# Kernel tuning notes

Measured on AMD Instinct MI355X. Metric: run time of the kernel, lower is better.

The kernel has to match this reference:

```python
import math
import jax, jax.numpy as jnp
import numpy as np

DIM = 1024
HID = 2048  # dim * expansion_factor
QK = 128
G = 256  # group size
NUM_BUCKETS = 32
MAX_DIST = 128
SCALE = QK ** 0.5


def t5_rel_bias(rel_emb, g):
    # non-causal T5 relative position bias over a g x g window
    pos = jnp.arange(g)
    n = pos[:, None] - pos[None, :]  # n = -(k - q) = q - k
    nb = NUM_BUCKETS // 2  # 16
    ret = (n < 0).astype(jnp.int32) * nb
    n = jnp.abs(n)
    max_exact = nb // 2  # 8
    is_small = n < max_exact
    val_large = max_exact + (
        jnp.log(jnp.maximum(n, 1).astype(jnp.float32) / max_exact)
        / math.log(MAX_DIST / max_exact) * (nb - max_exact)
    ).astype(jnp.int32)
    val_large = jnp.minimum(val_large, nb - 1)
    bucket = ret + jnp.where(is_small, n, val_large)
    return rel_emb[bucket, 0] * SCALE  # [g, g]


def setup_inputs() -> dict:
    key = jax.random.key(0)
    ks = jax.random.split(key, 8)
    d = {}
    d['x'] = jax.random.normal(ks[0], (4, 4096, DIM), dtype=jnp.float32)
    d['ln_g'] = jnp.ones((DIM,), jnp.float32)
    d['ln_b'] = jnp.zeros((DIM,), jnp.float32)
    d['W_h'] = jax.random.normal(ks[1], (DIM, 2 * HID), jnp.float32) * (1.0 / math.sqrt(DIM))
    d['b_h'] = jnp.zeros((2 * HID,), jnp.float32)
    d['W_qk'] = jax.random.normal(ks[2], (DIM, QK), jnp.float32) * (1.0 / math.sqrt(DIM))
    d['b_qk'] = jnp.zeros((QK,), jnp.float32)
    d['os_g'] = 1.0 + 0.02 * jax.random.normal(ks[3], (4, QK), jnp.float32)
    d['os_b'] = jnp.zeros((4, QK), jnp.float32)
    d['rel_emb'] = jax.random.normal(ks[4], (NUM_BUCKETS, 1), jnp.float32)
    d['W_o'] = jax.random.normal(ks[5], (HID, DIM), jnp.float32) * (1.0 / math.sqrt(HID))
    d['b_o'] = jnp.zeros((DIM,), jnp.float32)
    return d


def reference(x, ln_g, ln_b, W_h, b_h, W_qk, b_qk, os_g, os_b, rel_emb, W_o, b_o):
    b, n, _ = x.shape
    # LayerNorm
    mu = jnp.mean(x, axis=-1, keepdims=True)
    var = jnp.var(x, axis=-1, keepdims=True)
    normed = (x - mu) * jax.lax.rsqrt(var + 1e-5) * ln_g + ln_b
    # to_hidden -> v, gate ; to_qk
    hidden = jax.nn.silu(normed @ W_h + b_h)  # [b, n, 2*HID]
    v, gate = hidden[..., :HID], hidden[..., HID:]
    qk = jax.nn.silu(normed @ W_qk + b_qk)  # [b, n, QK]
    # offset-scale into 4 heads
    heads = qk[..., None, :] * os_g + os_b  # [b, n, 4, QK]
    quad_q, lin_q, quad_k, lin_k = [heads[..., h, :] for h in range(4)]
    # group: n divisible by G (no padding needed)
    ng = n // G
    grp = lambda t: t.reshape(b, ng, G, -1)
    quad_q, quad_k, lin_q, lin_k, vg = map(grp, (quad_q, quad_k, lin_q, lin_k, v))
    # grouped quadratic attention with ReLU^2 and T5 bias
    sim = jnp.einsum('bgid,bgjd->bgij', quad_q, quad_k) / G
    sim = sim + t5_rel_bias(rel_emb, G)
    attn = jnp.square(jax.nn.relu(sim))
    quad_out = jnp.einsum('bgij,bgjd->bgid', attn, vg)
    # linear attention, reduced over groups (non-causal)
    lin_kv = jnp.einsum('bgnd,bgne->bde', lin_k, vg) / n
    lin_out = jnp.einsum('bgnd,bde->bgne', lin_q, lin_kv)
    out = gate * (quad_out.reshape(b, n, HID) + lin_out.reshape(b, n, HID))
    return out @ W_o + b_o + x
```

## Files before the change

### kernel.cpp

```cpp
#include <hip/hip_runtime.h>
#include <hip/hip_bf16.h>

typedef float  f32x4  __attribute__((ext_vector_type(4)));
typedef __bf16 bf16x8 __attribute__((ext_vector_type(8)));
typedef __bf16 bf16x4 __attribute__((ext_vector_type(4)));

__device__ __forceinline__ float silu_f(float x) { return x / (1.0f + __expf(-x)); }

__device__ __forceinline__ void gload16(const __bf16* g, const char* lds) {
    __builtin_amdgcn_global_load_lds((const __attribute__((address_space(1))) void*)g,
                                     (__attribute__((address_space(3))) void*)lds, 16, 0, 0);
}

__global__ __launch_bounds__(256) void prepln_kernel(const float* __restrict__ x,
                                                     const float* __restrict__ ln_g,
                                                     const float* __restrict__ ln_b,
                                                     __bf16* __restrict__ norm,
                                                     const float* __restrict__ W_h,
                                                     const float* __restrict__ W_qk,
                                                     const float* __restrict__ W_o,
                                                     const float* __restrict__ rel_emb,
                                                     __bf16* __restrict__ WhT,
                                                     __bf16* __restrict__ WqkT,
                                                     __bf16* __restrict__ WoT,
                                                     float* __restrict__ bmat) {
    __shared__ float red[8];
    __shared__ __bf16 tile[32][33];
    int id = blockIdx.x, tid = threadIdx.x;
    if (id < 16384) {
        const float* xr = x + (long)id * 1024;
        f32x4 v = *(const f32x4*)(xr + tid * 4);
        float s  = v[0] + v[1] + v[2] + v[3];
        float ss = v[0]*v[0] + v[1]*v[1] + v[2]*v[2] + v[3]*v[3];
        #pragma unroll
        for (int off = 32; off > 0; off >>= 1) {
            s  += __shfl_down(s, off);
            ss += __shfl_down(ss, off);
        }
        int wave = tid >> 6, lane = tid & 63;
        if (lane == 0) { red[wave*2] = s; red[wave*2+1] = ss; }
        __syncthreads();
        float S  = red[0] + red[2] + red[4] + red[6];
        float SS = red[1] + red[3] + red[5] + red[7];
        float mean = S * (1.0f/1024.0f);
        float var  = SS * (1.0f/1024.0f) - mean*mean;
        float rstd = rsqrtf(var + 1e-5f);
        __bf16* orow = norm + (long)id * 1024;
        #pragma unroll
        for (int j = 0; j < 4; j++) {
            float fv = (v[j] - mean) * rstd * ln_g[tid*4+j] + ln_b[tid*4+j];
            orow[tid*4+j] = (__bf16)fv;
        }
        return;
    }
    id -= 16384;
    if (id >= 6272) {
        int idx = (id - 6272) * 256 + tid;
        int i = idx >> 8, j = idx & 255;
        int n = i - j;
        int ret = (n < 0) ? 16 : 0;
        int an = (n < 0) ? -n : n;
        int bucket;
        if (an < 8) {
            bucket = ret + an;
        } else {
            float vl = logf((float)an * 0.125f) / 2.772588722239781f * 8.0f;
            int lv = 8 + (int)vl;
            bucket = ret + (lv < 15 ? lv : 15);
        }
        bmat[idx] = rel_emb[bucket] * 11.313708498984761f;
        return;
    }
    const float* in; __bf16* outp; int rows, cols, tx, ty;
    if (id < 4096)      { in = W_h;  outp = WhT;  rows = 1024; cols = 4096; tx = id % 128; ty = id / 128; }
    else if (id < 4224) { int t = id - 4096; in = W_qk; outp = WqkT; rows = 1024; cols = 128;  tx = t % 4;  ty = t / 4; }
    else                { int t = id - 4224; in = W_o;  outp = WoT;  rows = 2048; cols = 1024; tx = t % 32; ty = t / 32; }
    int c0 = tx * 32, r0 = ty * 32;
    int lx = tid & 31, ly = tid >> 5;
    #pragma unroll
    for (int i = 0; i < 4; i++) {
        int r = ly + i*8;
        tile[r][lx] = (__bf16)in[(long)(r0 + r) * cols + c0 + lx];
    }
    __syncthreads();
    #pragma unroll
    for (int i = 0; i < 4; i++) {
        int c = ly + i*8;
        outp[(long)(c0 + c) * rows + r0 + lx] = tile[lx][c];
    }
}

__global__ __launch_bounds__(256) void reduce8_kernel(const __bf16* __restrict__ in,
                                                      __bf16* __restrict__ out) {
    int i = (blockIdx.x * 256 + threadIdx.x) * 4;
    int b = i >> 18;
    int r = i & 262143;
    float s0 = 0.f, s1 = 0.f, s2 = 0.f, s3 = 0.f;
    #pragma unroll
    for (int c = 0; c < 8; ++c) {
        bf16x4 v = *(const bf16x4*)(in + ((long)(b*8 + c) << 18) + r);
        s0 += (float)v[0]; s1 += (float)v[1]; s2 += (float)v[2]; s3 += (float)v[3];
    }
    bf16x4 o; o[0] = (__bf16)s0; o[1] = (__bf16)s1; o[2] = (__bf16)s2; o[3] = (__bf16)s3;
    *(bf16x4*)(out + i) = o;
}

struct GP {
    const __bf16* A;
    const __bf16* B;
    const __bf16* A2;
    const __bf16* B2;
    int lda, ldb, kSteps;
    long sAz, sBz, sCz;
    float scale;
    float* outF;
    __bf16 *o0, *o1, *o2, *o3, *o4, *o5;
    const float *c0, *c1, *c2, *c3;
    __bf16* gbuf;
};

__global__ __launch_bounds__(256, 2) void hqk_kernel(GP p) {
    __shared__ __bf16 As[2*128*32];
    __shared__ __bf16 Bs[2*128*32];
    int bx = blockIdx.x, by = blockIdx.y;
    bool qkm = (by == 32);
    const __bf16* A = p.A + (long)bx * 128 * 1024;
    const __bf16* B = qkm ? p.B2 : p.B + (long)by * 128 * 1024;
    int tid = threadIdx.x;
    int wave = tid >> 6, lane = tid & 63;
    int wr = (wave >> 1) * 64, wc = (wave & 1) * 64;
    int lr = lane & 15, kg = lane >> 4;

    f32x4 acc[4][4] = {};

    int lsub = lane >> 2;
    int scol = (lane & 3) * 8;
    const __bf16* Ag = A + scol + (long)(wave*32 + lsub) * 1024;
    const __bf16* Bg = B + scol + (long)(wave*32 + lsub) * 1024;
    const long s16 = 16 * 1024;
    __bf16* AsW = As + wave * 32 * 32;
    __bf16* BsW = Bs + wave * 32 * 32;

    for (int ks = 0; ks < 16; ++ks) {
        long k0 = (long)ks * 64;
        __syncthreads();
        gload16(Ag + k0,            (const char*)AsW);
        gload16(Ag + k0 + s16,      (const char*)(AsW + 16*32));
        gload16(Bg + k0,            (const char*)BsW);
        gload16(Bg + k0 + s16,      (const char*)(BsW + 16*32));
        gload16(Ag + k0 + 32,       (const char*)(AsW + 4096));
        gload16(Ag + k0 + 32 + s16, (const char*)(AsW + 4096 + 16*32));
        gload16(Bg + k0 + 32,       (const char*)(BsW + 4096));
        gload16(Bg + k0 + 32 + s16, (const char*)(BsW + 4096 + 16*32));
        __syncthreads();
#pragma unroll
        for (int kk = 0; kk < 2; ++kk) {
            bf16x8 af[4], bfr[4];
            #pragma unroll
            for (int i = 0; i < 4; i++) af[i]  = *(const bf16x8*)(As + kk*4096 + (wr + i*16 + lr)*32 + kg*8);
            #pragma unroll
            for (int i = 0; i < 4; i++) bfr[i] = *(const bf16x8*)(Bs + kk*4096 + (wc + i*16 + lr)*32 + kg*8);
            #pragma unroll
            for (int i = 0; i < 4; i++)
                #pragma unroll
                for (int j = 0; j < 4; j++)
                    acc[i][j] = __builtin_amdgcn_mfma_f32_16x16x32_bf16(af[i], bfr[j], acc[i][j], 0, 0, 0);
        }
    }

    #pragma unroll
    for (int i = 0; i < 4; i++) {
        #pragma unroll
        for (int j = 0; j < 4; j++) {
            int row0 = bx*128 + wr + i*16 + kg*4;
            if (!qkm) {
                int col = by*128 + wc + j*16 + lr;
                if (col < 2048) {
                    bf16x4 vv;
                    #pragma unroll
                    for (int q = 0; q < 4; q++) vv[q] = (__bf16)silu_f(acc[i][j][q] + p.c0[col]);
                    *(bf16x4*)(p.o0 + (long)col*16384 + row0) = vv;
                } else {
                    #pragma unroll
                    for (int q = 0; q < 4; q++)
                        p.o1[(long)(row0+q)*2048 + (col - 2048)] = (__bf16)silu_f(acc[i][j][q] + p.c0[col]);
                }
            } else {
                int col = wc + j*16 + lr;
                float sv[4];
                #pragma unroll
                for (int q = 0; q < 4; q++) sv[q] = silu_f(acc[i][j][q] + p.c3[col]);
                #pragma unroll
                for (int q = 0; q < 4; q++) {
                    p.o2[(long)(row0+q)*128 + col] = (__bf16)(sv[q] * p.c1[      col] + p.c2[      col]);
                    p.o3[(long)(row0+q)*128 + col] = (__bf16)(sv[q] * p.c1[256 + col] + p.c2[256 + col]);
                    p.o4[(long)(row0+q)*128 + col] = (__bf16)(sv[q] * p.c1[128 + col] + p.c2[128 + col]);
                }
                bf16x4 lk;
                #pragma unroll
                for (int q = 0; q < 4; q++) lk[q] = (__bf16)(sv[q] * p.c1[384 + col] + p.c2[384 + col]);
                *(bf16x4*)(p.o5 + (long)col*16384 + row0) = lk;
            }
        }
    }
}

__global__ __launch_bounds__(256, 2) void gemm64f_kernel(GP p) {
    __shared__ __bf16 As[2*128*32];
    __shared__ __bf16 Bs[2*128*32];
    const __bf16* A = p.A + (long)blockIdx.x * 128 * p.lda;
    const __bf16* B = p.B + (long)blockIdx.y * 128 * p.ldb;
    int tid = threadIdx.x;
    int wave = tid >> 6, lane = tid & 63;
    int wr = (wave >> 1) * 64, wc = (wave & 1) * 64;
    int lr = lane & 15, kg = lane >> 4;

    f32x4 acc[4][4] = {};

    int lsub = lane >> 2;
    int scol = (lane & 3) * 8;
    const __bf16* Ag = A + scol + (long)(wave*32 + lsub) * p.lda;
    const __bf16* Bg = B + scol + (long)(wave*32 + lsub) * p.ldb;
    long a16 = (long)16 * p.lda, b16 = (long)16 * p.ldb;
    __bf16* AsW = As + wave * 32 * 32;
    __bf16* BsW = Bs + wave * 32 * 32;

    for (int ks = 0; ks < p.kSteps; ++ks) {
        long k0 = (long)ks * 64;
        __syncthreads();
        gload16(Ag + k0,            (const char*)AsW);
        gload16(Ag + k0 + a16,      (const char*)(AsW + 16*32));
        gload16(Bg + k0,            (const char*)BsW);
        gload16(Bg + k0 + b16,      (const char*)(BsW + 16*32));
        gload16(Ag + k0 + 32,       (const char*)(AsW + 4096));
        gload16(Ag + k0 + 32 + a16, (const char*)(AsW + 4096 + 16*32));
        gload16(Bg + k0 + 32,       (const char*)(BsW + 4096));
        gload16(Bg + k0 + 32 + b16, (const char*)(BsW + 4096 + 16*32));
        __syncthreads();
#pragma unroll
        for (int kk = 0; kk < 2; ++kk) {
            bf16x8 af[4], bfr[4];
            #pragma unroll
            for (int i = 0; i < 4; i++) af[i]  = *(const bf16x8*)(As + kk*4096 + (wr + i*16 + lr)*32 + kg*8);
            #pragma unroll
            for (int i = 0; i < 4; i++) bfr[i] = *(const bf16x8*)(Bs + kk*4096 + (wc + i*16 + lr)*32 + kg*8);
            #pragma unroll
            for (int i = 0; i < 4; i++)
                #pragma unroll
                for (int j = 0; j < 4; j++)
                    acc[i][j] = __builtin_amdgcn_mfma_f32_16x16x32_bf16(af[i], bfr[j], acc[i][j], 0, 0, 0);
        }
    }

    int bx = blockIdx.x, by = blockIdx.y;
    #pragma unroll
    for (int i = 0; i < 4; i++) {
        #pragma unroll
        for (int j = 0; j < 4; j++) {
            int row0 = bx*128 + wr + i*16 + kg*4;
            int col  = by*128 + wc + j*16 + lr;
            #pragma unroll
            for (int q = 0; q < 4; q++) {
                long idx = (long)(row0+q)*1024 + col;
                p.outF[idx] = acc[i][j][q] + p.c0[col] + p.c1[idx];
            }
        }
    }
}

__global__ __launch_bounds__(256, 2) void simlinkv_kernel(GP ps, GP pl) {
    __shared__ __bf16 As[2*128*32];
    __shared__ __bf16 Bs[2*128*32];
    int id = blockIdx.x;
    bool sim = id < 256;
    GP p = sim ? ps : pl;
    int bx, by, z;
    if (sim) { bx = id & 1; by = (id >> 1) & 1; z = id >> 2; }
    else     { int t = id - 256; bx = 0; by = t & 15; z = t >> 4; }

    const __bf16* A = p.A + (long)z * p.sAz + (long)bx * 128 * p.lda;
    const __bf16* B = p.B + (long)z * p.sBz + (long)by * 128 * p.ldb;
    int tid = threadIdx.x;
    int wave = tid >> 6, lane = tid & 63;
    int wr = (wave >> 1) * 64, wc = (wave & 1) * 64;
    int lr = lane & 15, kg = lane >> 4;

    f32x4 acc[4][4] = {};

    int lsub = lane >> 2;
    int scol = (lane & 3) * 8;
    const __bf16* Ag = A + scol + (long)(wave*32 + lsub) * p.lda;
    const __bf16* Bg = B + scol + (long)(wave*32 + lsub) * p.ldb;
    long a16 = (long)16 * p.lda, b16 = (long)16 * p.ldb;
    __bf16* AsW = As + wave * 32 * 32;
    __bf16* BsW = Bs + wave * 32 * 32;

    for (int ks = 0; ks < p.kSteps; ++ks) {
        long k0 = (long)ks * 64;
        __syncthreads();
        gload16(Ag + k0,            (const char*)AsW);
        gload16(Ag + k0 + a16,      (const char*)(AsW + 16*32));
        gload16(Bg + k0,            (const char*)BsW);
        gload16(Bg + k0 + b16,      (const char*)(BsW + 16*32));
        gload16(Ag + k0 + 32,       (const char*)(AsW + 4096));
        gload16(Ag + k0 + 32 + a16, (const char*)(AsW + 4096 + 16*32));
        gload16(Bg + k0 + 32,       (const char*)(BsW + 4096));
        gload16(Bg + k0 + 32 + b16, (const char*)(BsW + 4096 + 16*32));
        __syncthreads();
#pragma unroll
        for (int kk = 0; kk < 2; ++kk) {
            bf16x8 af[4], bfr[4];
            #pragma unroll
            for (int i = 0; i < 4; i++) af[i]  = *(const bf16x8*)(As + kk*4096 + (wr + i*16 + lr)*32 + kg*8);
            #pragma unroll
            for (int i = 0; i < 4; i++) bfr[i] = *(const bf16x8*)(Bs + kk*4096 + (wc + i*16 + lr)*32 + kg*8);
            #pragma unroll
            for (int i = 0; i < 4; i++)
                #pragma unroll
                for (int j = 0; j < 4; j++)
                    acc[i][j] = __builtin_amdgcn_mfma_f32_16x16x32_bf16(af[i], bfr[j], acc[i][j], 0, 0, 0);
        }
    }

    #pragma unroll
    for (int i = 0; i < 4; i++) {
        #pragma unroll
        for (int j = 0; j < 4; j++) {
            int row0 = bx*128 + wr + i*16 + kg*4;
            int col  = by*128 + wc + j*16 + lr;
            if (sim) {
                #pragma unroll
                for (int q = 0; q < 4; q++) {
                    int row = row0 + q;
                    float s = acc[i][j][q] * (1.0f/256.0f) + p.c0[row*256 + col];
                    s = fmaxf(s, 0.0f);
                    p.o0[(long)z*p.sCz + (long)row*256 + col] = (__bf16)(s * s);
                }
            } else {
                bf16x4 vv;
                #pragma unroll
                for (int q = 0; q < 4; q++) vv[q] = (__bf16)(acc[i][j][q] * p.scale);
                *(bf16x4*)(p.o0 + (long)z*p.sCz + (long)col*128 + row0) = vv;
            }
        }
    }
}

__global__ __launch_bounds__(256, 2) void quadlin_kernel(GP p) {
    __shared__ __bf16 As[2*128*32];
    __shared__ __bf16 Bs[2*128*32];
    int z = blockIdx.z;
    int batch = z >> 4;
    int tid = threadIdx.x;
    int wave = tid >> 6, lane = tid & 63;
    int wr = (wave >> 1) * 64, wc = (wave & 1) * 64;
    int lr = lane & 15, kg = lane >> 4;
    int lsub = lane >> 2;
    int scol = (lane & 3) * 8;
    __bf16* AsW = As + wave * 32 * 32;
    __bf16* BsW = Bs + wave * 32 * 32;

    f32x4 acc[4][4] = {};

    {
        const __bf16* Ag = p.A + (long)z * 65536 + (long)blockIdx.x * 128 * 256
                         + scol + (long)(wave*32 + lsub) * 256;
        const __bf16* Bg = p.B + (long)z * 256 + (long)blockIdx.y * 128 * 16384
                         + scol + (long)(wave*32 + lsub) * 16384;
        const long a16 = 16*256, b16 = 16L*16384;
        for (int ks = 0; ks < 4; ++ks) {
            long k0 = (long)ks * 64;
            __syncthreads();
            gload16(Ag + k0,            (const char*)AsW);
            gload16(Ag + k0 + a16,      (const char*)(AsW + 16*32));
            gload16(Bg + k0,            (const char*)BsW);
            gload16(Bg + k0 + b16,      (const char*)(BsW + 16*32));
            gload16(Ag + k0 + 32,       (const char*)(AsW + 4096));
            gload16(Ag + k0 + 32 + a16, (const char*)(AsW + 4096 + 16*32));
            gload16(Bg + k0 + 32,       (const char*)(BsW + 4096));
            gload16(Bg + k0 + 32 + b16, (const char*)(BsW + 4096 + 16*32));
            __syncthreads();
#pragma unroll
            for (int kk = 0; kk < 2; ++kk) {
                bf16x8 af[4], bfr[4];
                #pragma unroll
                for (int i = 0; i < 4; i++) af[i]  = *(const bf16x8*)(As + kk*4096 + (wr + i*16 + lr)*32 + kg*8);
                #pragma unroll
                for (int i = 0; i < 4; i++) bfr[i] = *(const bf16x8*)(Bs + kk*4096 + (wc + i*16 + lr)*32 + kg*8);
                #pragma unroll
                for (int i = 0; i < 4; i++)
                    #pragma unroll
                    for (int j = 0; j < 4; j++)
                        acc[i][j] = __builtin_amdgcn_mfma_f32_16x16x32_bf16(af[i], bfr[j], acc[i][j], 0, 0, 0);
            }
        }
    }
    {
        const __bf16* Ag = p.A2 + ((long)z * 256 + (long)blockIdx.x * 128) * 128
                         + scol + (long)(wave*32 + lsub) * 128;
        const __bf16* Bg = p.B2 + (long)batch * 2048 * 128 + (long)blockIdx.y * 128 * 128
                         + scol + (long)(wave*32 + lsub) * 128;
        const long a16 = 16*128, b16 = 16*128;
        for (int ks = 0; ks < 2; ++ks) {
            long k0 = (long)ks * 64;
            __syncthreads();
            gload16(Ag + k0,            (const char*)AsW);
            gload16(Ag + k0 + a16,      (const char*)(AsW + 16*32));
            gload16(Bg + k0,            (const char*)BsW);
            gload16(Bg + k0 + b16,      (const char*)(BsW + 16*32));
            gload16(Ag + k0 + 32,       (const char*)(AsW + 4096));
            gload16(Ag + k0 + 32 + a16, (const char*)(AsW + 4096 + 16*32));
            gload16(Bg + k0 + 32,       (const char*)(BsW + 4096));
            gload16(Bg + k0 + 32 + b16, (const char*)(BsW + 4096 + 16*32));
            __syncthreads();
#pragma unroll
            for (int kk = 0; kk < 2; ++kk) {
                bf16x8 af[4], bfr[4];
                #pragma unroll
                for (int i = 0; i < 4; i++) af[i]  = *(const bf16x8*)(As + kk*4096 + (wr + i*16 + lr)*32 + kg*8);
                #pragma unroll
                for (int i = 0; i < 4; i++) bfr[i] = *(const bf16x8*)(Bs + kk*4096 + (wc + i*16 + lr)*32 + kg*8);
                #pragma unroll
                for (int i = 0; i < 4; i++)
                    #pragma unroll
                    for (int j = 0; j < 4; j++)
                        acc[i][j] = __builtin_amdgcn_mfma_f32_16x16x32_bf16(af[i], bfr[j], acc[i][j], 0, 0, 0);
            }
        }
    }
    #pragma unroll
    for (int i = 0; i < 4; i++) {
        #pragma unroll
        for (int j = 0; j < 4; j++) {
            int row0 = z*256 + blockIdx.x*128 + wr + i*16 + kg*4;
            int col  = blockIdx.y*128 + wc + j*16 + lr;
            #pragma unroll
            for (int q = 0; q < 4; q++) {
                long idx = (long)(row0+q)*2048 + col;
                float g = (float)p.gbuf[idx];
                p.gbuf[idx] = (__bf16)(g * acc[i][j][q]);
            }
        }
    }
}

extern "C" void kernel_launch(void* const* d_in, const int* in_sizes, int n_in,
                              void* d_out, int out_size, void* d_ws, size_t ws_size,
                              hipStream_t stream) {
    const float* x       = (const float*)d_in[0];
    const float* ln_g    = (const float*)d_in[1];
    const float* ln_b    = (const float*)d_in[2];
    const float* W_h     = (const float*)d_in[3];
    const float* b_h     = (const float*)d_in[4];
    const float* W_qk    = (const float*)d_in[5];
    const float* b_qk    = (const float*)d_in[6];
    const float* os_g    = (const float*)d_in[7];
    const float* os_b    = (const float*)d_in[8];
    const float* rel_emb = (const float*)d_in[9];
    const float* W_o     = (const float*)d_in[10];
    const float* b_o     = (const float*)d_in[11];
    float* out = (float*)d_out;

    const size_t MB = 1024 * 1024;
    if (ws_size < 190 * MB) return;

    char* ws = (char*)d_ws;
    __bf16* gate = (__bf16*)(ws + 0);
    __bf16* vT   = (__bf16*)(ws + 64*MB);
    __bf16* norm = (__bf16*)(ws + 128*MB);
    __bf16* attn = (__bf16*)(ws + 128*MB);
    __bf16* lkvT = (__bf16*)(ws + 136*MB);
    __bf16* lkvP = (__bf16*)(ws + 140*MB);
    __bf16* qq   = (__bf16*)(ws + 160*MB);
    __bf16* qk2  = (__bf16*)(ws + 164*MB);
    __bf16* lq   = (__bf16*)(ws + 168*MB);
    __bf16* lkT  = (__bf16*)(ws + 172*MB);
    float*  bmat = (float* )(ws + 176*MB);
    __bf16* WqkT = (__bf16*)(ws + 176*MB + 256*1024);
    __bf16* WoT  = (__bf16*)(ws + 177*MB);
    __bf16* WhT  = (__bf16*)(ws + 181*MB);

    prepln_kernel<<<22912, 256, 0, stream>>>(x, ln_g, ln_b, norm,
                                             W_h, W_qk, W_o, rel_emb,
                                             WhT, WqkT, WoT, bmat);

    {
        GP p{}; p.A = norm; p.B = WhT; p.B2 = WqkT;
        p.c0 = b_h; p.o0 = vT; p.o1 = gate;
        p.c3 = b_qk; p.c1 = os_g; p.c2 = os_b;
        p.o2 = qq; p.o3 = qk2; p.o4 = lq; p.o5 = lkT;
        hqk_kernel<<<dim3(128, 33), 256, 0, stream>>>(p);
    }
    {
        GP ps{}; ps.A = qq; ps.B = qk2; ps.lda = 128; ps.ldb = 128; ps.kSteps = 2;
        ps.sAz = 256*128; ps.sBz = 256*128; ps.sCz = 256*256;
        ps.c0 = bmat; ps.o0 = attn;
        GP pl{}; pl.A = lkT; pl.B = vT; pl.lda = 16384; pl.ldb = 16384; pl.kSteps = 8;
        pl.sAz = 512; pl.sBz = 512; pl.sCz = 2048*128; pl.scale = 1.0f/4096.0f;
        pl.o0 = lkvP;
        simlinkv_kernel<<<768, 256, 0, stream>>>(ps, pl);
    }
    reduce8_kernel<<<1024, 256, 0, stream>>>(lkvP, lkvT);
    {
        GP p{}; p.A = attn; p.B = vT; p.A2 = lq; p.B2 = lkvT; p.gbuf = gate;
        quadlin_kernel<<<dim3(2, 16, 64), 256, 0, stream>>>(p);
    }
    {
        GP p{}; p.A = gate; p.B = WoT; p.lda = 2048; p.ldb = 2048; p.kSteps = 32;
        p.c0 = b_o; p.c1 = x; p.outF = out;
        gemm64f_kernel<<<dim3(128, 8), 256, 0, stream>>>(p);
    }
}
```

Measured before the change: 412.1 us.

## Merge hidden/qk and output GEMMs into templated 256x128 tile kernel

Replaces the two 128x128-tile GEMM kernels with one templated kernel that computes 256x128 output tiles. Each wave now owns 64 rows across all 128 columns, with a 4x8 accumulator array. This raises arithmetic intensity per LDS load and halves the grid size for the hidden/qk projection and the output projection. In exchange it doubles accumulator registers, drops the occupancy hint of 2, and leaves fewer blocks, for example 512 for the output GEMM, which risks under-filling the GPU.

Result: slower. 743.5 us (+80.4%).

```diff
diff --git a/kernel.cpp b/kernel.cpp
--- a/kernel.cpp
+++ b/kernel.cpp
@@ -119,150 +119,101 @@
     __bf16* gbuf;
 };
 
-__global__ __launch_bounds__(256, 2) void hqk_kernel(GP p) {
-    __shared__ __bf16 As[2*128*32];
+template<int EPI>
+__global__ __launch_bounds__(256) void g256x128_kernel(GP p) {
+    __shared__ __bf16 As[2*256*32];
     __shared__ __bf16 Bs[2*128*32];
     int bx = blockIdx.x, by = blockIdx.y;
-    bool qkm = (by == 32);
-    const __bf16* A = p.A + (long)bx * 128 * 1024;
-    const __bf16* B = qkm ? p.B2 : p.B + (long)by * 128 * 1024;
+    const bool qkm = (EPI == 0) && (by == 32);
+    const __bf16* A = p.A + (long)bx * 256 * p.lda;
+    const __bf16* B = qkm ? p.B2 : p.B + (long)by * 128 * p.ldb;
     int tid = threadIdx.x;
     int wave = tid >> 6, lane = tid & 63;
-    int wr = (wave >> 1) * 64, wc = (wave & 1) * 64;
     int lr = lane & 15, kg = lane >> 4;
 
-    f32x4 acc[4][4] = {};
+    f32x4 acc[4][8] = {};
 
     int lsub = lane >> 2;
     int scol = (lane & 3) * 8;
-    const __bf16* Ag = A + scol + (long)(wave*32 + lsub) * 1024;
-    const __bf16* Bg = B + scol + (long)(wave*32 + lsub) * 1024;
-    const long s16 = 16 * 1024;
-    __bf16* AsW = As + wave * 32 * 32;
-    __bf16* BsW = Bs + wave * 32 * 32;
-
-    for (int ks = 0; ks < 16; ++ks) {
+    const __bf16* AgW = A + scol + (long)(wave*64 + lsub) * p.lda;
+    const __bf16* BgW = B + scol + (long)(wave*32 + lsub) * p.ldb;
+    const long lda = p.lda, ldb = p.ldb;
+
+    for (int ks = 0; ks < p.kSteps; ++ks) {
         long k0 = (long)ks * 64;
-        __syncthreads();
-        gload16(Ag + k0,            (const char*)AsW);
-        gload16(Ag + k0 + s16,      (const char*)(AsW + 16*32));
-        gload16(Bg + k0,            (const char*)BsW);
-        gload16(Bg + k0 + s16,      (const char*)(BsW + 16*32));
-        gload16(Ag + k0 + 32,       (const char*)(AsW + 4096));
-        gload16(Ag + k0 + 32 + s16, (const char*)(AsW + 4096 + 16*32));
-        gload16(Bg + k0 + 32,       (const char*)(BsW + 4096));
-        gload16(Bg + k0 + 32 + s16, (const char*)(BsW + 4096 + 16*32));
         __syncthreads();
 #pragma unroll
         for (int kk = 0; kk < 2; ++kk) {
-            bf16x8 af[4], bfr[4];
-            #pragma unroll
-            for (int i = 0; i < 4; i++) af[i]  = *(const bf16x8*)(As + kk*4096 + (wr + i*16 + lr)*32 + kg*8);
-            #pragma unroll
-            for (int i = 0; i < 4; i++) bfr[i] = *(const bf16x8*)(Bs + kk*4096 + (wc + i*16 + lr)*32 + kg*8);
-            #pragma unroll
-            for (int i = 0; i < 4; i++)
-                #pragma unroll
-                for (int j = 0; j < 4; j++)
-                    acc[i][j] = __builtin_amdgcn_mfma_f32_16x16x32_bf16(af[i], bfr[j], acc[i][j], 0, 0, 0);
-        }
-    }
-
-    #pragma unroll
-    for (int i = 0; i < 4; i++) {
-        #pragma unroll
-        for (int j = 0; j < 4; j++) {
-            int row0 = bx*128 + wr + i*16 + kg*4;
-            if (!qkm) {
-                int col = by*128 + wc + j*16 + lr;
-                if (col < 2048) {
-                    bf16x4 vv;
-                    #pragma unroll
-                    for (int q = 0; q < 4; q++) vv[q] = (__bf16)silu_f(acc[i][j][q] + p.c0[col]);
-                    *(bf16x4*)(p.o0 + (long)col*16384 + row0) = vv;
-                } else {
-                    #pragma unroll
-                    for (int q = 0; q < 4; q++)
-                        p.o1[(long)(row0+q)*2048 + (col - 2048)] = (__bf16)silu_f(acc[i][j][q] + p.c0[col]);
-                }
-            } else {
-                int col = wc + j*16 + lr;
-                float sv[4];
-                #pragma unroll
-                for (int q = 0; q < 4; q++) sv[q] = silu_f(acc[i][j][q] + p.c3[col]);
-                #pragma unroll
-                for (int q = 0; q < 4; q++) {
-                    p.o2[(long)(row0+q)*128 + col] = (__bf16)(sv[q] * p.c1[      col] + p.c2[      col]);
-                    p.o3[(long)(row0+q)*128 + col] = (__bf16)(sv[q] * p.c1[256 + col] + p.c2[256 + col]);
-                    p.o4[(long)(row0+q)*128 + col] = (__bf16)(sv[q] * p.c1[128 + col] + p.c2[128 + col]);
-                }
-                bf16x4 lk;
-                #pragma unroll
-                for (int q = 0; q < 4; q++) lk[q] = (__bf16)(sv[q] * p.c1[384 + col] + p.c2[384 + col]);
-                *(bf16x4*)(p.o5 + (long)col*16384 + row0) = lk;
-            }
-        }
-    }
-}
-
-__global__ __launch_bounds__(256, 2) void gemm64f_kernel(GP p) {
-    __shared__ __bf16 As[2*128*32];
-    __shared__ __bf16 Bs[2*128*32];
-    const __bf16* A = p.A + (long)blockIdx.x * 128 * p.lda;
-    const __bf16* B = p.B + (long)blockIdx.y * 128 * p.ldb;
-    int tid = threadIdx.x;
-    int wave = tid >> 6, lane = tid & 63;
-    int wr = (wave >> 1) * 64, wc = (wave & 1) * 64;
-    int lr = lane & 15, kg = lane >> 4;
-
-    f32x4 acc[4][4] = {};
-
-    int lsub = lane >> 2;
-    int scol = (lane & 3) * 8;
-    const __bf16* Ag = A + scol + (long)(wave*32 + lsub) * p.lda;
-    const __bf16* Bg = B + scol + (long)(wave*32 + lsub) * p.ldb;
-    long a16 = (long)16 * p.lda, b16 = (long)16 * p.ldb;
-    __bf16* AsW = As + wave * 32 * 32;
-    __bf16* BsW = Bs + wave * 32 * 32;
-
-    for (int ks = 0; ks < p.kSteps; ++ks) {
-        long k0 = (long)ks * 64;
-        __syncthreads();
-        gload16(Ag + k0,            (const char*)AsW);
-        gload16(Ag + k0 + a16,      (const char*)(AsW + 16*32));
-        gload16(Bg + k0,            (const char*)BsW);
-        gload16(Bg + k0 + b16,      (const char*)(BsW + 16*32));
-        gload16(Ag + k0 + 32,       (const char*)(AsW + 4096));
-        gload16(Ag + k0 + 32 + a16, (const char*)(AsW + 4096 + 16*32));
-        gload16(Bg + k0 + 32,       (const char*)(BsW + 4096));
-        gload16(Bg + k0 + 32 + b16, (const char*)(BsW + 4096 + 16*32));
+            const __bf16* sA = AgW + k0 + kk*32;
+            const char* dA = (const char*)As + kk*16384 + wave*4096;
+            gload16(sA,           dA);
+            gload16(sA + 16*lda,  dA + 1024);
+            gload16(sA + 32*lda,  dA + 2048);
+            gload16(sA + 48*lda,  dA + 3072);
+            const __bf16* sB = BgW + k0 + kk*32;
+            const char* dB = (const char*)Bs + kk*8192 + wave*2048;
+            gload16(sB,           dB);
+            gload16(sB + 16*ldb,  dB + 1024);
+        }
         __syncthreads();
 #pragma unroll
         for (int kk = 0; kk < 2; ++kk) {
-            bf16x8 af[4], bfr[4];
-            #pragma unroll
-            for (int i = 0; i < 4; i++) af[i]  = *(const bf16x8*)(As + kk*4096 + (wr + i*16 + lr)*32 + kg*8);
-            #pragma unroll
-            for (int i = 0; i < 4; i++) bfr[i] = *(const bf16x8*)(Bs + kk*4096 + (wc + i*16 + lr)*32 + kg*8);
+            bf16x8 af[4], bfr[8];
             #pragma unroll
             for (int i = 0; i < 4; i++)
-                #pragma unroll
-                for (int j = 0; j < 4; j++)
+                af[i] = *(const bf16x8*)(As + kk*8192 + (wave*64 + i*16 + lr)*32 + kg*8);
+            #pragma unroll
+            for (int j = 0; j < 8; j++)
+                bfr[j] = *(const bf16x8*)(Bs + kk*4096 + (j*16 + lr)*32 + kg*8);
+            #pragma unroll
+            for (int i = 0; i < 4; i++)
+                #pragma unroll
+                for (int j = 0; j < 8; j++)
                     acc[i][j] = __builtin_amdgcn_mfma_f32_16x16x32_bf16(af[i], bfr[j], acc[i][j], 0, 0, 0);
         }
     }
 
-    int bx = blockIdx.x, by = blockIdx.y;
     #pragma unroll
     for (int i = 0; i < 4; i++) {
         #pragma unroll
-        for (int j = 0; j < 4; j++) {
-            int row0 = bx*128 + wr + i*16 + kg*4;
-            int col  = by*128 + wc + j*16 + lr;
-            #pragma unroll
-            for (int q = 0; q < 4; q++) {
-                long idx = (long)(row0+q)*1024 + col;
-                p.outF[idx] = acc[i][j][q] + p.c0[col] + p.c1[idx];
+        for (int j = 0; j < 8; j++) {
+            int row0 = bx*256 + wave*64 + i*16 + kg*4;
+            if constexpr (EPI == 0) {
+                if (!qkm) {
+                    int col = by*128 + j*16 + lr;
+                    if (col < 2048) {
+                        bf16x4 vv;
+                        #pragma unroll
+                        for (int q = 0; q < 4; q++) vv[q] = (__bf16)silu_f(acc[i][j][q] + p.c0[col]);
+                        *(bf16x4*)(p.o0 + (long)col*16384 + row0) = vv;
+                    } else {
+                        #pragma unroll
+                        for (int q = 0; q < 4; q++)
+                            p.o1[(long)(row0+q)*2048 + (col - 2048)] = (__bf16)silu_f(acc[i][j][q] + p.c0[col]);
+                    }
+                } else {
+                    int col = j*16 + lr;
+                    float sv[4];
+                    #pragma unroll
+                    for (int q = 0; q < 4; q++) sv[q] = silu_f(acc[i][j][q] + p.c3[col]);
+                    #pragma unroll
+                    for (int q = 0; q < 4; q++) {
+                        p.o2[(long)(row0+q)*128 + col] = (__bf16)(sv[q] * p.c1[      col] + p.c2[      col]);
+                        p.o3[(long)(row0+q)*128 + col] = (__bf16)(sv[q] * p.c1[256 + col] + p.c2[256 + col]);
+                        p.o4[(long)(row0+q)*128 + col] = (__bf16)(sv[q] * p.c1[128 + col] + p.c2[128 + col]);
+                    }
+                    bf16x4 lk;
+                    #pragma unroll
+                    for (int q = 0; q < 4; q++) lk[q] = (__bf16)(sv[q] * p.c1[384 + col] + p.c2[384 + col]);
+                    *(bf16x4*)(p.o5 + (long)col*16384 + row0) = lk;
+                }
+            } else {
+                int col = by*128 + j*16 + lr;
+                #pragma unroll
+                for (int q = 0; q < 4; q++) {
+                    long idx = (long)(row0+q)*1024 + col;
+                    p.outF[idx] = acc[i][j][q] + p.c0[col] + p.c1[idx];
+                }
             }
         }
     }
@@ -485,11 +436,11 @@
                                              WhT, WqkT, WoT, bmat);
 
     {
-        GP p{}; p.A = norm; p.B = WhT; p.B2 = WqkT;
+        GP p{}; p.A = norm; p.B = WhT; p.B2 = WqkT; p.lda = 1024; p.ldb = 1024; p.kSteps = 16;
         p.c0 = b_h; p.o0 = vT; p.o1 = gate;
         p.c3 = b_qk; p.c1 = os_g; p.c2 = os_b;
         p.o2 = qq; p.o3 = qk2; p.o4 = lq; p.o5 = lkT;
-        hqk_kernel<<<dim3(128, 33), 256, 0, stream>>>(p);
+        g256x128_kernel<0><<<dim3(64, 33), 256, 0, stream>>>(p);
     }
     {
         GP ps{}; ps.A = qq; ps.B = qk2; ps.lda = 128; ps.ldb = 128; ps.kSteps = 2;
@@ -508,6 +459,6 @@
     {
         GP p{}; p.A = gate; p.B = WoT; p.lda = 2048; p.ldb = 2048; p.kSteps = 32;
         p.c0 = b_o; p.c1 = x; p.outF = out;
-        gemm64f_kernel<<<dim3(128, 8), 256, 0, stream>>>(p);
-    }
-}
+        g256x128_kernel<6><<<dim3(64, 8), 256, 0, stream>>>(p);
+    }
+}
```
